# Kernel optimization log

Hardware: AMD Instinct MI355X
Metric: run time of the kernel (lower is better)

The kernel has to match this reference:

```python
import jax, jax.numpy as jnp
import numpy as np

RADIUS = 1.0
NSAMPLE = 32


def _query_ball(new_xyz, xyz, radius, nsample):
    # new_xyz (B,M,3), xyz (B,N,3) -> idx (B,M,nsample) int32
    B, M, _ = new_xyz.shape
    N = xyz.shape[1]
    # squared distances via ||q||^2 + ||p||^2 - 2 q.p (avoids BxMxNx3 diff tensor)
    q2 = jnp.sum(new_xyz * new_xyz, axis=-1)          # (B,M)
    p2 = jnp.sum(xyz * xyz, axis=-1)                  # (B,N)
    qp = jnp.einsum('bmd,bnd->bmn', new_xyz, xyz)     # (B,M,N)
    dist2 = q2[:, :, None] + p2[:, None, :] - 2.0 * qp
    mask = dist2 < radius * radius
    ar = jnp.arange(N, dtype=jnp.int32)
    masked = jnp.where(mask, ar[None, None, :], jnp.int32(N + 1))  # (B,M,N)
    first = jnp.sort(masked, axis=2)[:, :, :nsample]               # (B,M,S)
    first_valid = first[:, :, :1]                                   # pad with first neighbor
    idx = jnp.where(first == N + 1, first_valid, first)
    return idx.astype(jnp.int32)


def _group(points, idx):
    # points (B,C,N), idx (B,M,S) -> (B,C,M,S) gather along N
    B, C, N = points.shape
    M, S = idx.shape[1], idx.shape[2]
    ie = jnp.broadcast_to(idx.reshape(B, 1, M * S).astype(jnp.int32), (B, C, M * S))
    return jnp.take_along_axis(points, ie, axis=2).reshape(B, C, M, S)


def setup_inputs() -> dict:
    key = jax.random.key(0)
    k1, k2 = jax.random.split(key)
    B, N, M, C = 8, 8192, 2048, 64
    xyz = jax.random.normal(k1, (B, N, 3), dtype=jnp.float32)
    # centroids are a subset of the cloud -> every ball query has >= 1 valid neighbor
    new_xyz = xyz[:, :M, :]
    features = jax.random.normal(k2, (B, C, N), dtype=jnp.float32)
    return {"xyz": xyz, "new_xyz": new_xyz, "features": features}


def reference(xyz, new_xyz, features):
    idx = _query_ball(new_xyz, xyz, RADIUS, NSAMPLE)                      # (B,M,S)
    grouped_xyz = _group(jnp.swapaxes(xyz, 1, 2), idx)                    # (B,3,M,S)
    grouped_xyz = grouped_xyz - jnp.swapaxes(new_xyz, 1, 2)[..., None]    # recenter
    grouped_feat = _group(features, idx)                                  # (B,C,M,S)
    return jnp.concatenate([grouped_xyz, grouped_feat], axis=1)           # (B,3+C,M,S)
```

## Files before the change

### kernel.cpp

```cpp
#include <hip/hip_runtime.h>

#define N_PTS 8192
#define M_Q   2048
#define C_F   64
#define NS    32
#define B_SZ  8

__global__ __launch_bounds__(256) void prep_kernel(
    const float* __restrict__ feat, const float* __restrict__ xyz,
    float* __restrict__ featT, float4* __restrict__ xyz4)
{
#pragma clang fp contract(off)
    __shared__ float lds[C_F * 65];
    if (blockIdx.x < B_SZ * 128) {
        const int b  = blockIdx.x >> 7;
        const int n0 = (blockIdx.x & 127) * 64;
        {
            const int c4 = threadIdx.x >> 6;
            const int nn = threadIdx.x & 63;
#pragma unroll
            for (int k = 0; k < 16; ++k) {
                const int c = k * 4 + c4;
                lds[c * 65 + nn] = feat[((size_t)b * C_F + c) * N_PTS + n0 + nn];
            }
        }
        __syncthreads();
        {
            const int n4 = threadIdx.x >> 6;
            const int c  = threadIdx.x & 63;
#pragma unroll
            for (int k = 0; k < 16; ++k) {
                const int nn = k * 4 + n4;
                featT[((size_t)b * N_PTS + n0 + nn) * C_F + c] = lds[c * 65 + nn];
            }
        }
    } else {
        const int i = (blockIdx.x - B_SZ * 128) * 256 + (int)threadIdx.x;
        const float p0 = xyz[i * 3 + 0];
        const float p1 = xyz[i * 3 + 1];
        const float p2 = xyz[i * 3 + 2];
        const float s  = (p0 * p0 + p1 * p1) + p2 * p2;
        xyz4[i] = make_float4(p0, p1, p2, s);
    }
}

__global__ __launch_bounds__(256) void qbg_kernel(
    const float4* __restrict__ xyz4, const float* __restrict__ nxyz,
    const float* __restrict__ featT, float* __restrict__ out)
{
#pragma clang fp contract(off)
    __shared__ int   sidx[4][NS];
    __shared__ float stage[67 * 33];

    const int lane = threadIdx.x & 63;
    const int w    = threadIdx.x >> 6;
    const int q    = blockIdx.x * 4 + w;
    const int b    = q >> 11;
    const float4* __restrict__ xb = xyz4 + (size_t)b * N_PTS;

    {
        const float* __restrict__ qp = nxyz + (size_t)q * 3;
        const float qx = qp[0], qy = qp[1], qz = qp[2];
        const float q2 = (qx * qx + qy * qy) + qz * qz;

        int  cnt = 0;
        int  first_idx = 0;
        bool have_first = false;

        for (int base = 0; base < N_PTS && cnt < NS; base += 256) {
            float4 P[4];
#pragma unroll
            for (int cc = 0; cc < 4; ++cc)
                P[cc] = xb[base + cc * 64 + lane];
#pragma unroll
            for (int cc = 0; cc < 4; ++cc) {
                if (cnt >= NS) break;
                const float qpdot = (qx * P[cc].x + qy * P[cc].y) + qz * P[cc].z;
                const float d2 = (q2 + P[cc].w) - 2.0f * qpdot;
                const bool pred = d2 < 1.0f;
                const unsigned long long mask = __ballot(pred);
                if (mask) {
                    if (!have_first) {
                        first_idx = base + cc * 64 + __ffsll(mask) - 1;
                        have_first = true;
                    }
                    if (pred) {
                        const int pos = cnt + (int)__popcll(mask & ((1ull << lane) - 1ull));
                        if (pos < NS) sidx[w][pos] = base + cc * 64 + lane;
                    }
                    cnt += (int)__popcll(mask);
                }
            }
        }
        if (cnt < NS) {
            for (int p = cnt + lane; p < NS; p += 64) sidx[w][p] = first_idx;
        }
    }
    __syncthreads();

    const int pS = threadIdx.x >> 3;
    const int j  = threadIdx.x & 7;
    const size_t cstride = (size_t)M_Q * NS;

    for (int w2 = 0; w2 < 4; ++w2) {
        const int qq = blockIdx.x * 4 + w2;
        const int mm = qq & (M_Q - 1);
        const int n  = sidx[w2][pS];

        const float* __restrict__ fb = featT + ((size_t)b * N_PTS + n) * C_F;
#pragma unroll
        for (int k = 0; k < 2; ++k) {
            const int c = k * 32 + j * 4;
            const float4 v = *(const float4*)(fb + c);
            stage[(3 + c + 0) * 33 + pS] = v.x;
            stage[(3 + c + 1) * 33 + pS] = v.y;
            stage[(3 + c + 2) * 33 + pS] = v.z;
            stage[(3 + c + 3) * 33 + pS] = v.w;
        }
        if (j == 0) {
            const float4 pv = xb[n];
            const float* __restrict__ qp2 = nxyz + (size_t)qq * 3;
            stage[0 * 33 + pS] = pv.x - qp2[0];
            stage[1 * 33 + pS] = pv.y - qp2[1];
            stage[2 * 33 + pS] = pv.z - qp2[2];
        }
        __syncthreads();

        const size_t obase = ((size_t)b * 67 * M_Q + mm) * NS;
#pragma unroll
        for (int it = 0; it < 3; ++it) {
            const int e = it * 256 + (int)threadIdx.x;
            if (e < 67 * 8) {
                const int row  = e >> 3;
                const int col4 = (e & 7) * 4;
                float4 v;
                v.x = stage[row * 33 + col4 + 0];
                v.y = stage[row * 33 + col4 + 1];
                v.z = stage[row * 33 + col4 + 2];
                v.w = stage[row * 33 + col4 + 3];
                *(float4*)&out[obase + (size_t)row * cstride + col4] = v;
            }
        }
        __syncthreads();
    }
}

extern "C" void kernel_launch(void* const* d_in, const int* in_sizes, int n_in,
                              void* d_out, int out_size, void* d_ws, size_t ws_size,
                              hipStream_t stream)
{
    const float* xyz  = (const float*)d_in[0];
    const float* nxyz = (const float*)d_in[1];
    const float* feat = (const float*)d_in[2];
    float* out = (float*)d_out;

    float*  featT = (float*)d_ws;
    float4* xyz4  = (float4*)((char*)d_ws + (20 << 20));

    const int Q = B_SZ * M_Q;

    prep_kernel<<<B_SZ * 128 + (B_SZ * N_PTS) / 256, 256, 0, stream>>>(
        feat, xyz, featT, xyz4);
    qbg_kernel<<<Q / 4, 256, 0, stream>>>(xyz4, nxyz, featT, out);
}
```

Baseline: 178.2 us.

## Vectorize transpose, prefetch xyz and gather loads, use nontemporal output stores

The feature transpose kernel now reads and writes float4 instead of scalars. The ball-query scan software-prefetches the next 256 points while testing the current ones. The gather loop prefetches the next query's feature rows before the barrier and writes output with nontemporal stores. Together these aim to hide global load latency and cut cache pollution from the large streamed output, at the cost of more registers and possibly lower occupancy.

```diff
diff --git a/kernel.cpp b/kernel.cpp
--- a/kernel.cpp
+++ b/kernel.cpp
@@ -5,6 +5,8 @@
 #define C_F   64
 #define NS    32
 #define B_SZ  8
+
+typedef float f32x4 __attribute__((ext_vector_type(4)));
 
 __global__ __launch_bounds__(256) void prep_kernel(
     const float* __restrict__ feat, const float* __restrict__ xyz,
@@ -16,22 +18,32 @@
         const int b  = blockIdx.x >> 7;
         const int n0 = (blockIdx.x & 127) * 64;
         {
-            const int c4 = threadIdx.x >> 6;
-            const int nn = threadIdx.x & 63;
-#pragma unroll
-            for (int k = 0; k < 16; ++k) {
-                const int c = k * 4 + c4;
-                lds[c * 65 + nn] = feat[((size_t)b * C_F + c) * N_PTS + n0 + nn];
+            const int c_lo = (int)threadIdx.x >> 4;
+            const int n4   = ((int)threadIdx.x & 15) * 4;
+#pragma unroll
+            for (int k = 0; k < 4; ++k) {
+                const int c = k * 16 + c_lo;
+                const float4 v =
+                    *(const float4*)&feat[((size_t)b * C_F + c) * N_PTS + n0 + n4];
+                lds[c * 65 + n4 + 0] = v.x;
+                lds[c * 65 + n4 + 1] = v.y;
+                lds[c * 65 + n4 + 2] = v.z;
+                lds[c * 65 + n4 + 3] = v.w;
             }
         }
         __syncthreads();
         {
-            const int n4 = threadIdx.x >> 6;
-            const int c  = threadIdx.x & 63;
-#pragma unroll
-            for (int k = 0; k < 16; ++k) {
-                const int nn = k * 4 + n4;
-                featT[((size_t)b * N_PTS + n0 + nn) * C_F + c] = lds[c * 65 + nn];
+            const int n_lo = (int)threadIdx.x >> 4;
+            const int c0   = ((int)threadIdx.x & 15) * 4;
+#pragma unroll
+            for (int k = 0; k < 4; ++k) {
+                const int nn = k * 16 + n_lo;
+                float4 w;
+                w.x = lds[(c0 + 0) * 65 + nn];
+                w.y = lds[(c0 + 1) * 65 + nn];
+                w.z = lds[(c0 + 2) * 65 + nn];
+                w.w = lds[(c0 + 3) * 65 + nn];
+                *(float4*)&featT[((size_t)b * N_PTS + n0 + nn) * C_F + c0] = w;
             }
         }
     } else {
@@ -67,11 +79,16 @@
         int  first_idx = 0;
         bool have_first = false;
 
+        float4 P[4], Q[4];
+#pragma unroll
+        for (int cc = 0; cc < 4; ++cc) P[cc] = xb[cc * 64 + lane];
+
         for (int base = 0; base < N_PTS && cnt < NS; base += 256) {
-            float4 P[4];
-#pragma unroll
-            for (int cc = 0; cc < 4; ++cc)
-                P[cc] = xb[base + cc * 64 + lane];
+            const int nb = base + 256;
+            if (nb < N_PTS) {
+#pragma unroll
+                for (int cc = 0; cc < 4; ++cc) Q[cc] = xb[nb + cc * 64 + lane];
+            }
 #pragma unroll
             for (int cc = 0; cc < 4; ++cc) {
                 if (cnt >= NS) break;
@@ -91,6 +108,8 @@
                     cnt += (int)__popcll(mask);
                 }
             }
+#pragma unroll
+            for (int cc = 0; cc < 4; ++cc) P[cc] = Q[cc];
         }
         if (cnt < NS) {
             for (int p = cnt + lane; p < NS; p += 64) sidx[w][p] = first_idx;
@@ -102,30 +121,54 @@
     const int j  = threadIdx.x & 7;
     const size_t cstride = (size_t)M_Q * NS;
 
+    float4 va, vb, pv;
+    float q0v = 0.f, q1v = 0.f, q2v = 0.f;
+    {
+        const int n0 = sidx[0][pS];
+        const float* __restrict__ fb = featT + ((size_t)b * N_PTS + n0) * C_F;
+        va = *(const float4*)(fb + j * 4);
+        vb = *(const float4*)(fb + 32 + j * 4);
+        if (j == 0) {
+            pv = xb[n0];
+            const float* __restrict__ qp2 = nxyz + (size_t)(blockIdx.x * 4) * 3;
+            q0v = qp2[0]; q1v = qp2[1]; q2v = qp2[2];
+        }
+    }
+
     for (int w2 = 0; w2 < 4; ++w2) {
+        const int ca = j * 4;
+        stage[(3 + ca + 0)  * 33 + pS] = va.x;
+        stage[(3 + ca + 1)  * 33 + pS] = va.y;
+        stage[(3 + ca + 2)  * 33 + pS] = va.z;
+        stage[(3 + ca + 3)  * 33 + pS] = va.w;
+        stage[(35 + ca + 0) * 33 + pS] = vb.x;
+        stage[(35 + ca + 1) * 33 + pS] = vb.y;
+        stage[(35 + ca + 2) * 33 + pS] = vb.z;
+        stage[(35 + ca + 3) * 33 + pS] = vb.w;
+        if (j == 0) {
+            stage[0 * 33 + pS] = pv.x - q0v;
+            stage[1 * 33 + pS] = pv.y - q1v;
+            stage[2 * 33 + pS] = pv.z - q2v;
+        }
+
+        float4 van, vbn, pvn;
+        float q0n = 0.f, q1n = 0.f, q2n = 0.f;
+        if (w2 < 3) {
+            const int nx = sidx[w2 + 1][pS];
+            const float* __restrict__ fb = featT + ((size_t)b * N_PTS + nx) * C_F;
+            van = *(const float4*)(fb + j * 4);
+            vbn = *(const float4*)(fb + 32 + j * 4);
+            if (j == 0) {
+                pvn = xb[nx];
+                const float* __restrict__ qp2 =
+                    nxyz + (size_t)(blockIdx.x * 4 + w2 + 1) * 3;
+                q0n = qp2[0]; q1n = qp2[1]; q2n = qp2[2];
+            }
+        }
+        __syncthreads();
+
         const int qq = blockIdx.x * 4 + w2;
         const int mm = qq & (M_Q - 1);
-        const int n  = sidx[w2][pS];
-
-        const float* __restrict__ fb = featT + ((size_t)b * N_PTS + n) * C_F;
-#pragma unroll
-        for (int k = 0; k < 2; ++k) {
-            const int c = k * 32 + j * 4;
-            const float4 v = *(const float4*)(fb + c);
-            stage[(3 + c + 0) * 33 + pS] = v.x;
-            stage[(3 + c + 1) * 33 + pS] = v.y;
-            stage[(3 + c + 2) * 33 + pS] = v.z;
-            stage[(3 + c + 3) * 33 + pS] = v.w;
-        }
-        if (j == 0) {
-            const float4 pv = xb[n];
-            const float* __restrict__ qp2 = nxyz + (size_t)qq * 3;
-            stage[0 * 33 + pS] = pv.x - qp2[0];
-            stage[1 * 33 + pS] = pv.y - qp2[1];
-            stage[2 * 33 + pS] = pv.z - qp2[2];
-        }
-        __syncthreads();
-
         const size_t obase = ((size_t)b * 67 * M_Q + mm) * NS;
 #pragma unroll
         for (int it = 0; it < 3; ++it) {
@@ -133,15 +176,19 @@
             if (e < 67 * 8) {
                 const int row  = e >> 3;
                 const int col4 = (e & 7) * 4;
-                float4 v;
+                f32x4 v;
                 v.x = stage[row * 33 + col4 + 0];
                 v.y = stage[row * 33 + col4 + 1];
                 v.z = stage[row * 33 + col4 + 2];
                 v.w = stage[row * 33 + col4 + 3];
-                *(float4*)&out[obase + (size_t)row * cstride + col4] = v;
+                __builtin_nontemporal_store(
+                    v, (f32x4*)&out[obase + (size_t)row * cstride + col4]);
             }
         }
         __syncthreads();
+
+        va = van; vb = vbn; pv = pvn;
+        q0v = q0n; q1v = q1n; q2v = q2n;
     }
 }
 
```

Result: slower. 184.2 us (+3.4%).
